# Optimization experiments

Measured on AMD Instinct MI355X. Metric: run time of the kernel, lower is better.

Reference implementation:

```python
import jax, jax.numpy as jnp
import numpy as np

# Faithful math: AlphaLayer(maxdim=1) builds the Delaunay complex with simplex
# filtration value = max pairwise Euclidean distance; BarcodePolyFeature(0, 2, 0)
# sums (death - birth)^2 over FINITE H0 bars. For this filtration, H0 births are
# all 0 and finite H0 deaths are exactly the Euclidean-MST edge lengths (the EMST
# is a subgraph of the Delaunay graph), so the feature equals
# sum over MST edges of squared edge length. We compute it with a vectorized
# Prim's algorithm (lax.scan over N-1 selection steps, vmapped over batch).

NCC = 2  # num_connected_components
EPS = 1e-8


def _batch_normalize(x):
    # per-sample, per-channel standardization over the points axis
    mu = x.mean(axis=1, keepdims=True)
    sd = x.std(axis=1, keepdims=True)
    return (x - mu) / (sd + EPS)


def _pairwise_sq(pts):
    # pts: [N, D] -> [N, N] squared Euclidean distances
    sq = jnp.sum(pts * pts, axis=-1)
    d2 = sq[:, None] + sq[None, :] - 2.0 * (pts @ pts.T)
    return jnp.maximum(d2, 0.0)


def _mst_sq_cost(pts):
    # sum of squared Euclidean MST edge lengths via Prim's algorithm
    d2 = _pairwise_sq(pts)          # [N, N]
    n = d2.shape[0]
    visited0 = jnp.zeros(n, dtype=bool).at[0].set(True)
    mind0 = d2[0]                   # min sq-distance from tree to each node

    def step(carry, _):
        mind, visited = carry
        masked = jnp.where(visited, jnp.inf, mind)
        j = jnp.argmin(masked)
        cost = mind[j]              # squared length of MST edge added
        visited = visited.at[j].set(True)
        mind = jnp.minimum(mind, d2[j])
        return (mind, visited), cost

    _, costs = jax.lax.scan(step, (mind0, visited0), None, length=n - 1)
    return costs.sum()


def setup_inputs() -> dict:
    key = jax.random.key(0)
    r = jax.random.normal(key, (16, 2048, 3), dtype=jnp.float32)
    return {"r": r}


def reference(r):
    chunks = jnp.split(r, NCC, axis=1)  # torch.chunk(r, dim=1, chunks=ncc)
    res = []
    for c in chunks:
        cn = _batch_normalize(c)                 # [B, N/ncc, D]
        per_sample = jax.vmap(_mst_sq_cost)(cn)  # [B]
        res.append(per_sample.mean())            # reduction='mean'
    return sum(res) / len(res)
```

## Files before the change

### kernel.cpp

```cpp
#include <hip/hip_runtime.h>
#include <math.h>
#include <stdint.h>


#define NSAMP   32
#define NPTS    1024
#define SBLK    8
#define NPN     128
#define TPB     1024
#define MAXRD   11
#define EMPTY64 0xFFFFFFFFFFFFFFFFull

typedef unsigned long long u64;

__device__ __forceinline__ u64 aload64(const u64* p) {
  return __hip_atomic_load(p, __ATOMIC_RELAXED, __HIP_MEMORY_SCOPE_AGENT);
}
__device__ __forceinline__ void astore64(u64* p, u64 v) {
  __hip_atomic_store(p, v, __ATOMIC_RELAXED, __HIP_MEMORY_SCOPE_AGENT);
}

__device__ __forceinline__ void sbar(int* cnt, int* sense, int& ls) {
  __syncthreads();
  if (threadIdx.x == 0) {
    ls ^= 1;
    const int prev =
        __hip_atomic_fetch_add(cnt, 1, __ATOMIC_ACQ_REL, __HIP_MEMORY_SCOPE_AGENT);
    if (prev == SBLK - 1) {
      __hip_atomic_store(cnt, 0, __ATOMIC_RELAXED, __HIP_MEMORY_SCOPE_AGENT);
      __hip_atomic_store(sense, ls, __ATOMIC_RELEASE, __HIP_MEMORY_SCOPE_AGENT);
    } else {
      while (__hip_atomic_load(sense, __ATOMIC_ACQUIRE,
                               __HIP_MEMORY_SCOPE_AGENT) != ls) {
        __builtin_amdgcn_s_sleep(2);
      }
    }
  }
  __syncthreads();
}

__device__ __forceinline__ void block_sum2(float& a, float& b, float* red) {
#pragma unroll
  for (int off = 32; off > 0; off >>= 1) {
    a += __shfl_xor(a, off, 64);
    b += __shfl_xor(b, off, 64);
  }
  __syncthreads();
  const int wid = threadIdx.x >> 6;
  if ((threadIdx.x & 63) == 0) { red[wid * 2] = a; red[wid * 2 + 1] = b; }
  __syncthreads();
  float ra = 0.f, rb = 0.f;
#pragma unroll
  for (int k = 0; k < 16; ++k) { ra += red[k * 2]; rb += red[k * 2 + 1]; }
  a = ra; b = rb;
}

__global__ __launch_bounds__(TPB) void topo_kernel(
    const float* __restrict__ r, u64* __restrict__ gw0, u64* __restrict__ gw1,
    int* __restrict__ bar, float* __restrict__ acc, int* __restrict__ done,
    float* __restrict__ out) {
  const int s    = blockIdx.x & 31;
  const int part = blockIdx.x >> 5;
  const int tid  = threadIdx.x;

  __shared__ float4 P[NPTS];
  __shared__ u64 Wl[NPTS];
  __shared__ short parentL[NPTS];
  __shared__ short rootL[NPTS];
  __shared__ float red[32];

  int* bcnt = bar + s * 32;
  int* bsen = bar + s * 32 + 16;
  u64* __restrict__ gws0 = gw0 + s * NPTS;
  u64* __restrict__ gws1 = gw1 + s * NPTS;

  const float* __restrict__ base = r + (size_t)s * (NPTS * 3);
  const float px = base[tid * 3 + 0];
  const float py = base[tid * 3 + 1];
  const float pz = base[tid * 3 + 2];
  float sx = px, sy = py, sz = pz, dm = 0.f;
  block_sum2(sx, sy, red);
  block_sum2(sz, dm, red);
  const float mx = sx * (1.f / NPTS), my = sy * (1.f / NPTS), mz = sz * (1.f / NPTS);
  const float ex = px - mx, ey = py - my, ez = pz - mz;
  float vx = ex * ex, vy = ey * ey, vz = ez * ez;
  dm = 0.f;
  block_sum2(vx, vy, red);
  block_sum2(vz, dm, red);
  const float ix = 1.f / (sqrtf(vx * (1.f / NPTS)) + 1e-8f);
  const float iy = 1.f / (sqrtf(vy * (1.f / NPTS)) + 1e-8f);
  const float iz = 1.f / (sqrtf(vz * (1.f / NPTS)) + 1e-8f);
  P[tid] = make_float4(ex * ix, ey * iy, ez * iz, __uint_as_float((unsigned)tid));

  if (tid < NPN) {
    astore64(&gws0[part * NPN + tid], EMPTY64);
    astore64(&gws1[part * NPN + tid], EMPTY64);
  }
  int ls = 0;
  sbar(bcnt, bsen, ls);

  float total = 0.f;
  const int g  = tid >> 5;
  const int sl = tid & 31;
  const int n0 = part * NPN + g * 4;

  for (int rd = 0; rd < MAXRD; ++rd) {
    u64* __restrict__ gwc = (rd & 1) ? gws1 : gws0;
    const u64 tag = (u64)(15 - rd) << 60;

    Wl[tid] = EMPTY64;
    __syncthreads();

    float mex[4], mey[4], mez[4]; unsigned mc[4];
#pragma unroll
    for (int n = 0; n < 4; ++n) {
      const float4 p = P[n0 + n];
      mex[n] = p.x; mey[n] = p.y; mez[n] = p.z; mc[n] = __float_as_uint(p.w);
    }
    float bd[4]; int bj[4];
#pragma unroll
    for (int n = 0; n < 4; ++n) { bd[n] = INFINITY; bj[n] = n0 + n; }
#pragma unroll 8
    for (int jj = 0; jj < 32; ++jj) {
      const int j = sl + (jj << 5);
      const float4 q = P[j];
      const unsigned qc = __float_as_uint(q.w);
#pragma unroll
      for (int n = 0; n < 4; ++n) {
        const float dx = mex[n] - q.x, dy = mey[n] - q.y, dz = mez[n] - q.z;
        float d2 = dx * dx + dy * dy + dz * dz;
        d2 = (qc == mc[n]) ? INFINITY : d2;
        if (d2 < bd[n]) { bd[n] = d2; bj[n] = j; }
      }
    }
#pragma unroll
    for (int off = 16; off > 0; off >>= 1) {
#pragma unroll
      for (int n = 0; n < 4; ++n) {
        const float od = __shfl_xor(bd[n], off, 64);
        const int   oj = __shfl_xor(bj[n], off, 64);
        if (od < bd[n] || (od == bd[n] && oj < bj[n])) { bd[n] = od; bj[n] = oj; }
      }
    }
    if (sl == 0) {
#pragma unroll
      for (int n = 0; n < 4; ++n) {
        if (bd[n] < INFINITY) {
          const int node = n0 + n, j = bj[n];
          const unsigned a = (unsigned)(node < j ? node : j);
          const unsigned b = (unsigned)(node < j ? j : node);
          const u64 key = tag | ((u64)__float_as_uint(bd[n]) << 20)
                        | (a << 10) | b;
          atomicMin(&Wl[mc[n]], key);
        }
      }
    }
    __syncthreads();
    {
      const u64 w = Wl[tid];
      if (w != EMPTY64) atomicMin(&gwc[tid], w);
    }
    sbar(bcnt, bsen, ls);

    const u64 w = aload64(&gwc[tid]);
    Wl[tid] = w;
    __syncthreads();
    const unsigned curtag = (unsigned)(15 - rd);
    float wsum = 0.f;
    short par = (short)tid;
    if ((unsigned)(w >> 60) == curtag) {
      const int pmin = (int)((w >> 10) & 1023u);
      const int pmax = (int)(w & 1023u);
      const int cmin = (int)__float_as_uint(P[pmin].w);
      const int cmax = (int)__float_as_uint(P[pmax].w);
      const int c2 = (cmin == tid) ? cmax : cmin;
      par = (short)c2;
      const bool dup = (Wl[c2] == w);
      if (!dup || tid < c2)
        wsum = __uint_as_float((unsigned)((w >> 20) & 0xFFFFFFFFull));
    }
    parentL[tid] = par;
    __syncthreads();
    {
      const int p = parentL[tid];
      if (p != tid && parentL[p] == tid && tid < p) parentL[tid] = (short)tid;
    }
    __syncthreads();
    {
      int p = parentL[tid];
      for (int it = 0; it < 1024 && parentL[p] != p; ++it) p = parentL[p];
      rootL[tid] = (short)p;
    }
    __syncthreads();
    const int newlab = rootL[(int)__float_as_uint(P[tid].w)];
    float fc = (newlab == tid) ? 1.f : 0.f;
    block_sum2(wsum, fc, red);
    P[tid].w = __uint_as_float((unsigned)newlab);
    total += wsum;
    if (fc == 1.f) break;
  }

  if (part == 0 && tid == 0) {
    atomicAdd(acc, total);
    const int old =
        __hip_atomic_fetch_add(done, 1, __ATOMIC_ACQ_REL, __HIP_MEMORY_SCOPE_AGENT);
    if (old == NSAMP - 1) {
      const float t =
          __hip_atomic_load(acc, __ATOMIC_ACQUIRE, __HIP_MEMORY_SCOPE_AGENT);
      __hip_atomic_store(out, t * (1.f / NSAMP), __ATOMIC_RELAXED,
                         __HIP_MEMORY_SCOPE_SYSTEM);
    }
  }
}

extern "C" void kernel_launch(void* const* d_in, const int* in_sizes, int n_in,
                              void* d_out, int out_size, void* d_ws, size_t ws_size,
                              hipStream_t stream) {
  const float* r = (const float*)d_in[0];
  float* out = (float*)d_out;
  (void)in_sizes; (void)n_in; (void)out_size; (void)ws_size;

  char* ws = (char*)d_ws;
  int*   bar  = (int*)ws;
  float* acc  = (float*)(ws + 4096);
  int*   done = (int*)(ws + 4100);
  u64*   gw0  = (u64*)(ws + 8192);
  u64*   gw1  = (u64*)(ws + 8192 + NSAMP * NPTS * sizeof(u64));

  hipMemsetAsync(ws, 0, 4160, stream);
  topo_kernel<<<dim3(NSAMP * SBLK), dim3(TPB), 0, stream>>>(
      r, gw0, gw1, bar, acc, done, out);
}
```

Baseline: 179.9 us.

## Replace sense-reversing grid barrier with per-block round flags and trim syncs

Swaps the counter/sense grid barrier for per-block monotonic round flags that thread 0 polls, and moves the global-buffer EMPTY initialization out of the kernel into a host memset, which removes the initial cross-block barrier. Pointer jumping for root finding is merged into one pass with 2-cycle detection, and the per-round block reductions are replaced by __syncthreads_count, with the total summed once at the end. Together these cut the barriers and global atomics per Boruvka round. The cost is an extra large memset launch, and the flag-polling protocol is harder to reason about.

```diff
diff --git a/kernel.cpp b/kernel.cpp
--- a/kernel.cpp
+++ b/kernel.cpp
@@ -15,28 +15,6 @@
 
 __device__ __forceinline__ u64 aload64(const u64* p) {
   return __hip_atomic_load(p, __ATOMIC_RELAXED, __HIP_MEMORY_SCOPE_AGENT);
-}
-__device__ __forceinline__ void astore64(u64* p, u64 v) {
-  __hip_atomic_store(p, v, __ATOMIC_RELAXED, __HIP_MEMORY_SCOPE_AGENT);
-}
-
-__device__ __forceinline__ void sbar(int* cnt, int* sense, int& ls) {
-  __syncthreads();
-  if (threadIdx.x == 0) {
-    ls ^= 1;
-    const int prev =
-        __hip_atomic_fetch_add(cnt, 1, __ATOMIC_ACQ_REL, __HIP_MEMORY_SCOPE_AGENT);
-    if (prev == SBLK - 1) {
-      __hip_atomic_store(cnt, 0, __ATOMIC_RELAXED, __HIP_MEMORY_SCOPE_AGENT);
-      __hip_atomic_store(sense, ls, __ATOMIC_RELEASE, __HIP_MEMORY_SCOPE_AGENT);
-    } else {
-      while (__hip_atomic_load(sense, __ATOMIC_ACQUIRE,
-                               __HIP_MEMORY_SCOPE_AGENT) != ls) {
-        __builtin_amdgcn_s_sleep(2);
-      }
-    }
-  }
-  __syncthreads();
 }
 
 __device__ __forceinline__ void block_sum2(float& a, float& b, float* red) {
@@ -56,9 +34,9 @@
 }
 
 __global__ __launch_bounds__(TPB) void topo_kernel(
-    const float* __restrict__ r, u64* __restrict__ gw0, u64* __restrict__ gw1,
-    int* __restrict__ bar, float* __restrict__ acc, int* __restrict__ done,
-    float* __restrict__ out) {
+    const float* __restrict__ r, u64* __restrict__ gw,
+    int* __restrict__ flags, float* __restrict__ acc,
+    int* __restrict__ done, float* __restrict__ out) {
   const int s    = blockIdx.x & 31;
   const int part = blockIdx.x >> 5;
   const int tid  = threadIdx.x;
@@ -66,50 +44,37 @@
   __shared__ float4 P[NPTS];
   __shared__ u64 Wl[NPTS];
   __shared__ short parentL[NPTS];
-  __shared__ short rootL[NPTS];
   __shared__ float red[32];
 
-  int* bcnt = bar + s * 32;
-  int* bsen = bar + s * 32 + 16;
-  u64* __restrict__ gws0 = gw0 + s * NPTS;
-  u64* __restrict__ gws1 = gw1 + s * NPTS;
+  int* fl = flags + s * 32;
+  u64* __restrict__ gws0 = gw + s * NPTS;
+  u64* __restrict__ gws1 = gw + (NSAMP + s) * NPTS;
 
   const float* __restrict__ base = r + (size_t)s * (NPTS * 3);
   const float px = base[tid * 3 + 0];
   const float py = base[tid * 3 + 1];
   const float pz = base[tid * 3 + 2];
   float sx = px, sy = py, sz = pz, dm = 0.f;
-  block_sum2(sx, sy, red);
-  block_sum2(sz, dm, red);
+  block_sum2(sx, sy, red); block_sum2(sz, dm, red);
   const float mx = sx * (1.f / NPTS), my = sy * (1.f / NPTS), mz = sz * (1.f / NPTS);
   const float ex = px - mx, ey = py - my, ez = pz - mz;
   float vx = ex * ex, vy = ey * ey, vz = ez * ez;
   dm = 0.f;
-  block_sum2(vx, vy, red);
-  block_sum2(vz, dm, red);
+  block_sum2(vx, vy, red); block_sum2(vz, dm, red);
   const float ix = 1.f / (sqrtf(vx * (1.f / NPTS)) + 1e-8f);
   const float iy = 1.f / (sqrtf(vy * (1.f / NPTS)) + 1e-8f);
   const float iz = 1.f / (sqrtf(vz * (1.f / NPTS)) + 1e-8f);
   P[tid] = make_float4(ex * ix, ey * iy, ez * iz, __uint_as_float((unsigned)tid));
-
-  if (tid < NPN) {
-    astore64(&gws0[part * NPN + tid], EMPTY64);
-    astore64(&gws1[part * NPN + tid], EMPTY64);
-  }
-  int ls = 0;
-  sbar(bcnt, bsen, ls);
+  Wl[tid] = EMPTY64;
+  __syncthreads();
 
   float total = 0.f;
-  const int g  = tid >> 5;
-  const int sl = tid & 31;
+  const int g  = tid >> 5, sl = tid & 31;
   const int n0 = part * NPN + g * 4;
 
   for (int rd = 0; rd < MAXRD; ++rd) {
     u64* __restrict__ gwc = (rd & 1) ? gws1 : gws0;
     const u64 tag = (u64)(15 - rd) << 60;
-
-    Wl[tid] = EMPTY64;
-    __syncthreads();
 
     float mex[4], mey[4], mez[4]; unsigned mc[4];
 #pragma unroll
@@ -145,28 +110,43 @@
     if (sl == 0) {
 #pragma unroll
       for (int n = 0; n < 4; ++n) {
-        if (bd[n] < INFINITY) {
-          const int node = n0 + n, j = bj[n];
-          const unsigned a = (unsigned)(node < j ? node : j);
-          const unsigned b = (unsigned)(node < j ? j : node);
-          const u64 key = tag | ((u64)__float_as_uint(bd[n]) << 20)
-                        | (a << 10) | b;
-          atomicMin(&Wl[mc[n]], key);
+        const int node = n0 + n, j = bj[n];
+        const unsigned a = (unsigned)(node < j ? node : j);
+        const unsigned b = (unsigned)(node < j ? j : node);
+        const u64 key = tag | ((u64)__float_as_uint(bd[n]) << 20)
+                      | (a << 10) | b;
+        atomicMin(&Wl[mc[n]], key);
+      }
+    }
+    __syncthreads();
+    if (sl == 0) {
+#pragma unroll
+      for (int n = 0; n < 4; ++n) atomicMin(&gwc[mc[n]], Wl[mc[n]]);
+    }
+
+    __syncthreads();
+    if (tid == 0) {
+      __hip_atomic_store(&fl[part], rd + 1, __ATOMIC_RELEASE,
+                         __HIP_MEMORY_SCOPE_AGENT);
+      for (;;) {
+        int mn = 0x7fffffff;
+#pragma unroll
+        for (int b2 = 0; b2 < SBLK; ++b2) {
+          const int v = __hip_atomic_load(&fl[b2], __ATOMIC_ACQUIRE,
+                                          __HIP_MEMORY_SCOPE_AGENT);
+          mn = v < mn ? v : mn;
         }
-      }
-    }
-    __syncthreads();
-    {
-      const u64 w = Wl[tid];
-      if (w != EMPTY64) atomicMin(&gwc[tid], w);
-    }
-    sbar(bcnt, bsen, ls);
+        if (mn >= rd + 1) break;
+        __builtin_amdgcn_s_sleep(1);
+      }
+    }
+    __syncthreads();
 
     const u64 w = aload64(&gwc[tid]);
     Wl[tid] = w;
     __syncthreads();
     const unsigned curtag = (unsigned)(15 - rd);
-    float wsum = 0.f;
+    float wadd = 0.f;
     short par = (short)tid;
     if ((unsigned)(w >> 60) == curtag) {
       const int pmin = (int)((w >> 10) & 1023u);
@@ -177,38 +157,41 @@
       par = (short)c2;
       const bool dup = (Wl[c2] == w);
       if (!dup || tid < c2)
-        wsum = __uint_as_float((unsigned)((w >> 20) & 0xFFFFFFFFull));
+        wadd = __uint_as_float((unsigned)((w >> 20) & 0xFFFFFFFFull));
     }
     parentL[tid] = par;
     __syncthreads();
+    int c = (int)__float_as_uint(P[tid].w);
     {
-      const int p = parentL[tid];
-      if (p != tid && parentL[p] == tid && tid < p) parentL[tid] = (short)tid;
-    }
-    __syncthreads();
-    {
-      int p = parentL[tid];
-      for (int it = 0; it < 1024 && parentL[p] != p; ++it) p = parentL[p];
-      rootL[tid] = (short)p;
-    }
-    __syncthreads();
-    const int newlab = rootL[(int)__float_as_uint(P[tid].w)];
-    float fc = (newlab == tid) ? 1.f : 0.f;
-    block_sum2(wsum, fc, red);
-    P[tid].w = __uint_as_float((unsigned)newlab);
-    total += wsum;
-    if (fc == 1.f) break;
+      int prev = -1, p = c;
+      for (int it = 0; it < 1024; ++it) {
+        const int nx = parentL[p];
+        if (nx == p) break;
+        if (nx == prev) { p = p < prev ? p : prev; break; }
+        prev = p; p = nx;
+      }
+      c = p;
+    }
+    total += wadd;
+    const int cnt = __syncthreads_count(c == tid);
+    P[tid].w = __uint_as_float((unsigned)c);
+    if (cnt == 1) break;
+    __syncthreads();
   }
 
-  if (part == 0 && tid == 0) {
-    atomicAdd(acc, total);
-    const int old =
-        __hip_atomic_fetch_add(done, 1, __ATOMIC_ACQ_REL, __HIP_MEMORY_SCOPE_AGENT);
-    if (old == NSAMP - 1) {
-      const float t =
-          __hip_atomic_load(acc, __ATOMIC_ACQUIRE, __HIP_MEMORY_SCOPE_AGENT);
-      __hip_atomic_store(out, t * (1.f / NSAMP), __ATOMIC_RELAXED,
-                         __HIP_MEMORY_SCOPE_SYSTEM);
+  {
+    float tt = total, dm2 = 0.f;
+    block_sum2(tt, dm2, red);
+    if (part == 0 && tid == 0) {
+      atomicAdd(acc, tt);
+      const int old = __hip_atomic_fetch_add(done, 1, __ATOMIC_ACQ_REL,
+                                             __HIP_MEMORY_SCOPE_AGENT);
+      if (old == NSAMP - 1) {
+        const float t = __hip_atomic_load(acc, __ATOMIC_ACQUIRE,
+                                          __HIP_MEMORY_SCOPE_AGENT);
+        __hip_atomic_store(out, t * (1.f / NSAMP), __ATOMIC_RELAXED,
+                           __HIP_MEMORY_SCOPE_SYSTEM);
+      }
     }
   }
 }
@@ -221,13 +204,13 @@
   (void)in_sizes; (void)n_in; (void)out_size; (void)ws_size;
 
   char* ws = (char*)d_ws;
-  int*   bar  = (int*)ws;
-  float* acc  = (float*)(ws + 4096);
-  int*   done = (int*)(ws + 4100);
-  u64*   gw0  = (u64*)(ws + 8192);
-  u64*   gw1  = (u64*)(ws + 8192 + NSAMP * NPTS * sizeof(u64));
-
-  hipMemsetAsync(ws, 0, 4160, stream);
+  int*   flags = (int*)ws;
+  float* acc   = (float*)(ws + 4096);
+  int*   done  = (int*)(ws + 4100);
+  u64*   gw    = (u64*)(ws + 8192);
+
+  hipMemsetAsync(ws, 0, 4104, stream);
+  hipMemsetAsync(ws + 8192, 0xFF, 2 * NSAMP * NPTS * sizeof(u64), stream);
   topo_kernel<<<dim3(NSAMP * SBLK), dim3(TPB), 0, stream>>>(
-      r, gw0, gw1, bar, acc, done, out);
-}
+      r, gw, flags, acc, done, out);
+}
```

Result: slower. 222.3 us (+23.6%).
